# Performance work log

Measured on AMD Instinct MI355X. Metric: run time of the kernel, lower is better.

The kernel has to match this reference:

```python
import jax, jax.numpy as jnp
import numpy as np

B, Q = 4096, 1024   # batch, time-series length
L, K = 64, 32       # num shapelets, shapelet length


def setup_inputs() -> dict:
    key = jax.random.key(0)
    k1, k2, k3, k4 = jax.random.split(key, 4)
    return {
        "ts": jax.random.normal(k1, (B, Q), dtype=jnp.float32),
        "shapelets": jax.random.normal(k2, (L, K), dtype=jnp.float32),
        "fc_w": jax.random.normal(k3, (2, L), dtype=jnp.float32) * 0.1,
        "fc_b": jax.random.normal(k4, (2,), dtype=jnp.float32) * 0.1,
    }


def reference(ts, shapelets, fc_w, fc_b):
    # Sliding-window mean squared distance, fused via the expansion
    #   mean((seg - s)^2) = (sum seg^2 - 2 seg.s + sum s^2) / K
    # which avoids materializing [B, L, S, K] windows.
    S = Q - K + 1  # number of segments

    # sliding sum of ts^2 over windows of length K -> [B, S]
    cs = jnp.concatenate([jnp.zeros((B, 1), ts.dtype), jnp.cumsum(ts * ts, axis=1)], axis=1)
    win_sq = cs[:, K:] - cs[:, :-K]

    # cross-correlation ts * shapelet -> [B, L, S] via a 1D valid conv
    cross = jax.lax.conv_general_dilated(
        ts[:, None, :],          # [B, 1, Q]  (NCW)
        shapelets[:, None, :],   # [L, 1, K]  (OIW)
        window_strides=(1,),
        padding="VALID",
        dimension_numbers=("NCW", "OIW", "NCW"),
    )

    shap_sq = jnp.sum(shapelets * shapelets, axis=1)  # [L]

    # [B, L, S] distance profile, then hard min over segment positions -> [B, L]
    dist = (win_sq[:, None, :] - 2.0 * cross + shap_sq[None, :, None]) / K
    feat = jnp.min(dist, axis=2)

    # fc1
    return feat @ fc_w.T + fc_b
```

## Files before the change

kernel.cpp:

```cpp
#include <hip/hip_runtime.h>
#include <stdint.h>

#define NB 4096
#define QLEN 1024
#define NL 64
#define KLEN 32
#define NS (QLEN - KLEN + 1)
#define WSLICE 1856

typedef __attribute__((ext_vector_type(8))) _Float16 half8;
typedef __attribute__((ext_vector_type(4))) float f32x4;

union fragh { uint32_t u[4]; half8 v; };

static __device__ __forceinline__ uint32_t pkh(float a, float b) {
    return __builtin_bit_cast(uint32_t, __builtin_amdgcn_cvt_pkrtz(a, b));
}
static __device__ __forceinline__ float lo16f(uint32_t w) {
    return (float)__builtin_bit_cast(_Float16, (unsigned short)(w & 0xFFFFu));
}
static __device__ __forceinline__ float hi16f(uint32_t w) {
    return (float)__builtin_bit_cast(_Float16, (unsigned short)(w >> 16));
}
static __device__ __forceinline__ uint32_t pkh_rne(float a, float b) {
    unsigned short ha = __builtin_bit_cast(unsigned short, (_Float16)a);
    unsigned short hb = __builtin_bit_cast(unsigned short, (_Float16)b);
    return (uint32_t)ha | ((uint32_t)hb << 16);
}

__global__ __launch_bounds__(256, 4) void shapelet_r15(
    const float* __restrict__ ts,
    const float* __restrict__ shapelets,
    const float* __restrict__ fc_w,
    const float* __restrict__ fc_b,
    float* __restrict__ out)
{
    __shared__ __align__(16) uint32_t lds[4 * WSLICE];

    const int tid  = threadIdx.x;
    const int wave = tid >> 6;
    const int lane = tid & 63;
    const int col  = lane & 15;
    const int kg   = lane >> 4;
    const int row  = blockIdx.x * 4 + wave;

    uint32_t* pkE = lds + wave * WSLICE;
    uint32_t* pkO = pkE + 528;
    uint32_t* nwh = pkO + 528;
    float*    s4  = reinterpret_cast<float*>(nwh + 512);

    const float* rowp = ts + (size_t)row * QLEN;
    float4 v[4];
    #pragma unroll
    for (int c = 0; c < 4; ++c)
        v[c] = reinterpret_cast<const float4*>(rowp)[64 * c + lane];
    float x4[4];
    #pragma unroll
    for (int c = 0; c < 4; ++c) {
        const int p = 256 * c + 4 * lane + 4;
        x4[c] = (p < QLEN) ? rowp[p] : 0.0f;
    }
    #pragma unroll
    for (int c = 0; c < 4; ++c) {
        uint2 pe = { pkh(v[c].x, v[c].y), pkh(v[c].z, v[c].w) };
        uint2 po = { pkh(v[c].y, v[c].z), pkh(v[c].w, x4[c]) };
        reinterpret_cast<uint2*>(pkE)[64 * c + lane] = pe;
        reinterpret_cast<uint2*>(pkO)[64 * c + lane] = po;
        s4[64 * c + lane] =
            fmaf(v[c].x, v[c].x, fmaf(v[c].y, v[c].y, fmaf(v[c].z, v[c].z, v[c].w * v[c].w)));
    }
    if (lane < 16) { pkE[512 + lane] = 0u; pkO[512 + lane] = 0u; }
    if (lane < 8)  s4[256 + lane] = 0.0f;

    fragh Bh[4];
    float ssq[4];
    #pragma unroll
    for (int lt = 0; lt < 4; ++lt) {
        const float* sp = shapelets + (lt * 16 + col) * KLEN + kg * 8;
        float4 f0 = *reinterpret_cast<const float4*>(sp);
        float4 f1 = *reinterpret_cast<const float4*>(sp + 4);
        Bh[lt].u[0] = pkh(f0.x, f0.y);
        Bh[lt].u[1] = pkh(f0.z, f0.w);
        Bh[lt].u[2] = pkh(f1.x, f1.y);
        Bh[lt].u[3] = pkh(f1.z, f1.w);
        float s = f0.x * f0.x;
        s = fmaf(f0.y, f0.y, s); s = fmaf(f0.z, f0.z, s); s = fmaf(f0.w, f0.w, s);
        s = fmaf(f1.x, f1.x, s); s = fmaf(f1.y, f1.y, s);
        s = fmaf(f1.z, f1.z, s); s = fmaf(f1.w, f1.w, s);
        ssq[lt] = s;
    }

    __builtin_amdgcn_wave_barrier();

    #pragma unroll
    for (int c = 0; c < 4; ++c) {
        const int q = 64 * c + lane;
        float s_[8];
        #pragma unroll
        for (int j = 0; j < 8; ++j) s_[j] = s4[q + j];
        float w0 = ((s_[0] + s_[1]) + (s_[2] + s_[3])) + ((s_[4] + s_[5]) + (s_[6] + s_[7]));
        uint32_t cw0 = pkE[2 * (q + 8)];
        uint32_t cw1 = pkE[2 * (q + 8) + 1];
        float x32 = lo16f(cw0), x33 = hi16f(cw0), x34 = lo16f(cw1);
        float w1 = fmaf(x32, x32, fmaf(-v[c].x, v[c].x, w0));
        float w2 = fmaf(x33, x33, fmaf(-v[c].y, v[c].y, w1));
        float w3 = fmaf(x34, x34, fmaf(-v[c].z, v[c].z, w2));
        const int p0 = 4 * q;
        float c0 = (p0 + 0 < NS) ? -0.5f * w0 : -60000.0f;
        float c1 = (p0 + 1 < NS) ? -0.5f * w1 : -60000.0f;
        float c2 = (p0 + 2 < NS) ? -0.5f * w2 : -60000.0f;
        float c3 = (p0 + 3 < NS) ? -0.5f * w3 : -60000.0f;
        const int qq = p0 & 31;
        const int W = ((p0 >> 5) << 4) + (((qq & 15) >> 2) << 2) + ((qq >> 4) << 1);
        uint2 hw = { pkh_rne(c0, c1), pkh_rne(c2, c3) };
        *reinterpret_cast<uint2*>(&nwh[W]) = hw;
    }

    __builtin_amdgcn_wave_barrier();

    float rmax[4][4];
    #pragma unroll
    for (int lt = 0; lt < 4; ++lt)
        #pragma unroll
        for (int e = 0; e < 4; ++e) rmax[lt][e] = -3.0e38f;

    const int par = col & 1;
    const uint32_t* apk = (par ? pkO : pkE) + (((col - par) >> 1) + kg * 4);
    const int nwb = 4 * kg;

    #pragma unroll 1
    for (int p = 0; p < 16; ++p) {
        const uint32_t* ap0 = apk + 32 * p;
        const uint32_t* ap1 = apk + 32 * p + 16;

        fragh Aa0, Ab0, Aa1, Ab1;
        #pragma unroll
        for (int j = 0; j < 4; ++j) Aa0.u[j] = ap0[j];
        #pragma unroll
        for (int j = 0; j < 4; ++j) Ab0.u[j] = ap0[8 + j];
        #pragma unroll
        for (int j = 0; j < 4; ++j) Aa1.u[j] = ap1[j];
        #pragma unroll
        for (int j = 0; j < 4; ++j) Ab1.u[j] = ap1[8 + j];
        uint4 nw0 = *reinterpret_cast<const uint4*>(&nwh[32 * p + nwb]);
        uint4 nw1 = *reinterpret_cast<const uint4*>(&nwh[32 * p + 16 + nwb]);

        f32x4 ia0, ib0, ia1, ib1;
        ia0[0] = lo16f(nw0.x); ia0[1] = hi16f(nw0.x);
        ia0[2] = lo16f(nw0.y); ia0[3] = hi16f(nw0.y);
        ib0[0] = lo16f(nw0.z); ib0[1] = hi16f(nw0.z);
        ib0[2] = lo16f(nw0.w); ib0[3] = hi16f(nw0.w);
        ia1[0] = lo16f(nw1.x); ia1[1] = hi16f(nw1.x);
        ia1[2] = lo16f(nw1.y); ia1[3] = hi16f(nw1.y);
        ib1[0] = lo16f(nw1.z); ib1[1] = hi16f(nw1.z);
        ib1[2] = lo16f(nw1.w); ib1[3] = hi16f(nw1.w);

        #pragma unroll
        for (int lt = 0; lt < 4; ++lt) {
            f32x4 aa0 = __builtin_amdgcn_mfma_f32_16x16x32_f16(Aa0.v, Bh[lt].v, ia0, 0, 0, 0);
            f32x4 ab0 = __builtin_amdgcn_mfma_f32_16x16x32_f16(Ab0.v, Bh[lt].v, ib0, 0, 0, 0);
            f32x4 aa1 = __builtin_amdgcn_mfma_f32_16x16x32_f16(Aa1.v, Bh[lt].v, ia1, 0, 0, 0);
            f32x4 ab1 = __builtin_amdgcn_mfma_f32_16x16x32_f16(Ab1.v, Bh[lt].v, ib1, 0, 0, 0);
            #pragma unroll
            for (int e = 0; e < 4; ++e) {
                rmax[lt][e] = fmaxf(fmaxf(aa0[e], ab0[e]), rmax[lt][e]);
                rmax[lt][e] = fmaxf(fmaxf(aa1[e], ab1[e]), rmax[lt][e]);
            }
        }
    }

    float p0v = 0.0f, p1v = 0.0f;
    #pragma unroll
    for (int lt = 0; lt < 4; ++lt) {
        float m = fmaxf(fmaxf(rmax[lt][0], rmax[lt][1]),
                        fmaxf(rmax[lt][2], rmax[lt][3]));
        m = fmaxf(m, __shfl_xor(m, 16, 64));
        m = fmaxf(m, __shfl_xor(m, 32, 64));
        float sq = ssq[lt];
        sq += __shfl_xor(sq, 16, 64);
        sq += __shfl_xor(sq, 32, 64);
        float f = (sq - 2.0f * m) * (1.0f / (float)KLEN);
        p0v = fmaf(f, fc_w[lt * 16 + col], p0v);
        p1v = fmaf(f, fc_w[NL + lt * 16 + col], p1v);
    }
    #pragma unroll
    for (int off = 1; off <= 8; off <<= 1) {
        p0v += __shfl_xor(p0v, off, 64);
        p1v += __shfl_xor(p1v, off, 64);
    }
    if (lane == 0) {
        out[(size_t)row * 2 + 0] = p0v + fc_b[0];
        out[(size_t)row * 2 + 1] = p1v + fc_b[1];
    }
}

extern "C" void kernel_launch(void* const* d_in, const int* in_sizes, int n_in,
                              void* d_out, int out_size, void* d_ws, size_t ws_size,
                              hipStream_t stream) {
    const float* ts        = (const float*)d_in[0];
    const float* shapelets = (const float*)d_in[1];
    const float* fc_w      = (const float*)d_in[2];
    const float* fc_b      = (const float*)d_in[3];
    float* out = (float*)d_out;

    shapelet_r15<<<NB / 4, 256, 0, stream>>>(ts, shapelets, fc_w, fc_b, out);
}
```

Before: 23.45 us.

## Store four shifted LDS copies of packed series for aligned 128-bit fragment loads

Each packed even/odd half-precision series is now written into LDS four times, each copy shifted by a different word offset. This lets every lane fetch its MFMA A fragment with one aligned 16-byte load instead of four scalar 32-bit loads. The launch also changes from 4 waves per 256-thread block to one 64-thread wave per block, one row each, with a larger per-wave LDS slice. The cost is extra LDS writes and footprint during setup, which may lower occupancy.

```diff
diff --git a/kernel.cpp b/kernel.cpp
--- a/kernel.cpp
+++ b/kernel.cpp
@@ -6,12 +6,18 @@
 #define NL 64
 #define KLEN 32
 #define NS (QLEN - KLEN + 1)
-#define WSLICE 1856
+
+#define ASTRIDE  528
+#define OFF_E0   0
+#define OFF_O0   (4 * ASTRIDE)
+#define OFF_NWH  (8 * ASTRIDE)
+#define OFF_S4   (OFF_NWH + 512)
+#define SLICE_SZ (OFF_S4 + 264)
 
 typedef __attribute__((ext_vector_type(8))) _Float16 half8;
 typedef __attribute__((ext_vector_type(4))) float f32x4;
 
-union fragh { uint32_t u[4]; half8 v; };
+union frag4 { uint4 q; half8 v; uint32_t u[4]; };
 
 static __device__ __forceinline__ uint32_t pkh(float a, float b) {
     return __builtin_bit_cast(uint32_t, __builtin_amdgcn_cvt_pkrtz(a, b));
@@ -28,33 +34,37 @@
     return (uint32_t)ha | ((uint32_t)hb << 16);
 }
 
-__global__ __launch_bounds__(256, 4) void shapelet_r15(
+__global__ __launch_bounds__(64, 2) void shapelet_r19(
     const float* __restrict__ ts,
     const float* __restrict__ shapelets,
     const float* __restrict__ fc_w,
     const float* __restrict__ fc_b,
     float* __restrict__ out)
 {
-    __shared__ __align__(16) uint32_t lds[4 * WSLICE];
-
-    const int tid  = threadIdx.x;
-    const int wave = tid >> 6;
-    const int lane = tid & 63;
+    __shared__ __align__(16) uint32_t lds[SLICE_SZ];
+
+    const int lane = threadIdx.x & 63;
     const int col  = lane & 15;
     const int kg   = lane >> 4;
-    const int row  = blockIdx.x * 4 + wave;
-
-    uint32_t* pkE = lds + wave * WSLICE;
-    uint32_t* pkO = pkE + 528;
-    uint32_t* nwh = pkO + 528;
-    float*    s4  = reinterpret_cast<float*>(nwh + 512);
+    const int row  = blockIdx.x;
+
+    uint32_t* E0 = lds + OFF_E0;
+    uint32_t* E1 = E0 + ASTRIDE;
+    uint32_t* E2 = E1 + ASTRIDE;
+    uint32_t* E3 = E2 + ASTRIDE;
+    uint32_t* O0 = lds + OFF_O0;
+    uint32_t* O1 = O0 + ASTRIDE;
+    uint32_t* O2 = O1 + ASTRIDE;
+    uint32_t* O3 = O2 + ASTRIDE;
+    uint32_t* nwh = lds + OFF_NWH;
+    float*    s4  = reinterpret_cast<float*>(lds + OFF_S4);
 
     const float* rowp = ts + (size_t)row * QLEN;
     float4 v[4];
+    float  x4[4];
     #pragma unroll
     for (int c = 0; c < 4; ++c)
         v[c] = reinterpret_cast<const float4*>(rowp)[64 * c + lane];
-    float x4[4];
     #pragma unroll
     for (int c = 0; c < 4; ++c) {
         const int p = 256 * c + 4 * lane + 4;
@@ -62,17 +72,35 @@
     }
     #pragma unroll
     for (int c = 0; c < 4; ++c) {
+        const int P = 128 * c + 2 * lane;
         uint2 pe = { pkh(v[c].x, v[c].y), pkh(v[c].z, v[c].w) };
         uint2 po = { pkh(v[c].y, v[c].z), pkh(v[c].w, x4[c]) };
-        reinterpret_cast<uint2*>(pkE)[64 * c + lane] = pe;
-        reinterpret_cast<uint2*>(pkO)[64 * c + lane] = po;
+        *reinterpret_cast<uint2*>(E0 + P) = pe;
+        E1[P - 1] = pe.x; E1[P] = pe.y;
+        *reinterpret_cast<uint2*>(E2 + P - 2) = pe;
+        E3[P - 3] = pe.x; E3[P - 2] = pe.y;
+        *reinterpret_cast<uint2*>(O0 + P) = po;
+        O1[P - 1] = po.x; O1[P] = po.y;
+        *reinterpret_cast<uint2*>(O2 + P - 2) = po;
+        O3[P - 3] = po.x; O3[P - 2] = po.y;
         s4[64 * c + lane] =
             fmaf(v[c].x, v[c].x, fmaf(v[c].y, v[c].y, fmaf(v[c].z, v[c].z, v[c].w * v[c].w)));
     }
-    if (lane < 16) { pkE[512 + lane] = 0u; pkO[512 + lane] = 0u; }
-    if (lane < 8)  s4[256 + lane] = 0.0f;
-
-    fragh Bh[4];
+    if (lane < 8) {
+        const int P = 512 + 2 * lane;
+        uint2 z = { 0u, 0u };
+        *reinterpret_cast<uint2*>(E0 + P) = z;
+        E1[P - 1] = 0u; E1[P] = 0u;
+        *reinterpret_cast<uint2*>(E2 + P - 2) = z;
+        E3[P - 3] = 0u; E3[P - 2] = 0u;
+        *reinterpret_cast<uint2*>(O0 + P) = z;
+        O1[P - 1] = 0u; O1[P] = 0u;
+        *reinterpret_cast<uint2*>(O2 + P - 2) = z;
+        O3[P - 3] = 0u; O3[P - 2] = 0u;
+    }
+    if (lane < 8) s4[256 + lane] = 0.0f;
+
+    frag4 Bh[4];
     float ssq[4];
     #pragma unroll
     for (int lt = 0; lt < 4; ++lt) {
@@ -99,8 +127,8 @@
         #pragma unroll
         for (int j = 0; j < 8; ++j) s_[j] = s4[q + j];
         float w0 = ((s_[0] + s_[1]) + (s_[2] + s_[3])) + ((s_[4] + s_[5]) + (s_[6] + s_[7]));
-        uint32_t cw0 = pkE[2 * (q + 8)];
-        uint32_t cw1 = pkE[2 * (q + 8) + 1];
+        uint32_t cw0 = E0[2 * (q + 8)];
+        uint32_t cw1 = E0[2 * (q + 8) + 1];
         float x32 = lo16f(cw0), x33 = hi16f(cw0), x34 = lo16f(cw1);
         float w1 = fmaf(x32, x32, fmaf(-v[c].x, v[c].x, w0));
         float w2 = fmaf(x33, x33, fmaf(-v[c].y, v[c].y, w1));
@@ -125,25 +153,21 @@
         for (int e = 0; e < 4; ++e) rmax[lt][e] = -3.0e38f;
 
     const int par = col & 1;
-    const uint32_t* apk = (par ? pkO : pkE) + (((col - par) >> 1) + kg * 4);
-    const int nwb = 4 * kg;
+    const int cc  = col >> 1;
+    const int r   = cc & 3;
+    const int aoff = (par ? OFF_O0 : OFF_E0) + r * ASTRIDE;
+    const uint4* fr  = reinterpret_cast<const uint4*>(lds + aoff + (cc + 4 * kg - r));
+    const uint4* nwp = reinterpret_cast<const uint4*>(nwh);
 
     #pragma unroll 1
     for (int p = 0; p < 16; ++p) {
-        const uint32_t* ap0 = apk + 32 * p;
-        const uint32_t* ap1 = apk + 32 * p + 16;
-
-        fragh Aa0, Ab0, Aa1, Ab1;
-        #pragma unroll
-        for (int j = 0; j < 4; ++j) Aa0.u[j] = ap0[j];
-        #pragma unroll
-        for (int j = 0; j < 4; ++j) Ab0.u[j] = ap0[8 + j];
-        #pragma unroll
-        for (int j = 0; j < 4; ++j) Aa1.u[j] = ap1[j];
-        #pragma unroll
-        for (int j = 0; j < 4; ++j) Ab1.u[j] = ap1[8 + j];
-        uint4 nw0 = *reinterpret_cast<const uint4*>(&nwh[32 * p + nwb]);
-        uint4 nw1 = *reinterpret_cast<const uint4*>(&nwh[32 * p + 16 + nwb]);
+        frag4 Aa0, Ab0, Aa1, Ab1;
+        Aa0.q = fr[8 * p + 0];
+        Ab0.q = fr[8 * p + 2];
+        Aa1.q = fr[8 * p + 4];
+        Ab1.q = fr[8 * p + 6];
+        uint4 nw0 = nwp[8 * p + kg];
+        uint4 nw1 = nwp[8 * p + 4 + kg];
 
         f32x4 ia0, ib0, ia1, ib1;
         ia0[0] = lo16f(nw0.x); ia0[1] = hi16f(nw0.x);
@@ -203,5 +227,5 @@
     const float* fc_b      = (const float*)d_in[3];
     float* out = (float*)d_out;
 
-    shapelet_r15<<<NB / 4, 256, 0, stream>>>(ts, shapelets, fc_w, fc_b, out);
-}
+    shapelet_r19<<<NB, 64, 0, stream>>>(ts, shapelets, fc_w, fc_b, out);
+}
```

Result: no change. 23.45 us (+0.0%).
